# Kernel optimization log

Measured on AMD Instinct MI355X. Metric: run time of the kernel, lower is better.

## Reference

```python
import jax, jax.numpy as jnp
import numpy as np

NEG_INF = -1.0e9  # matches masked_fill value in the torch source


def setup_inputs() -> dict:
    key = jax.random.key(0)
    k1, k2, k3, k4 = jax.random.split(key, 4)
    B, H, L, D = 4, 16, 2048, 64
    query = jax.random.normal(k1, (B, H, L, D), dtype=jnp.float32)
    key_t = jax.random.normal(k2, (B, H, L, D), dtype=jnp.float32)
    value = jax.random.normal(k3, (B, H, L, D), dtype=jnp.float32)
    attention_mask = jax.random.randint(k4, (B, L), 0, 2, dtype=jnp.int64)
    return {"query": query, "key": key_t, "value": value, "attention_mask": attention_mask}


def reference(query, key, value, attention_mask):
    d = query.shape[-1]
    scale = 1.0 / jnp.sqrt(jnp.asarray(d, dtype=query.dtype))
    # scores: [B, H, Lq, Lk]
    scores = jnp.einsum("bhqd,bhkd->bhqk", query, key) * scale
    # mask: [B, Lk] -> [B, 1, 1, Lk]; positions where mask == 0 get -1e9
    m = attention_mask[:, None, None, :]
    scores = jnp.where(m == 0, jnp.asarray(NEG_INF, dtype=scores.dtype), scores)
    attn = jax.nn.softmax(scores, axis=-1)
    return jnp.einsum("bhqk,bhkd->bhqd", attn, value)
```

## Files before the change

### kernel.cpp

```cpp
#include <hip/hip_runtime.h>
#include <hip/hip_bf16.h>
#include <stdint.h>

#define B_    4
#define H_    16
#define L_    2048
#define D_    64
#define BH_   64
#define NT_   32
#define MASKBIAS (-1.4426950408889634e9f)

typedef __attribute__((ext_vector_type(8))) short bf16x8;
typedef __attribute__((ext_vector_type(8))) unsigned short ushort8;
typedef __attribute__((ext_vector_type(4))) unsigned short ushort4v;
typedef __attribute__((ext_vector_type(4))) float f32x4;

__device__ __forceinline__ ushort f2bf(float f) {
  union { float f; uint32_t u; } x; x.f = f;
  uint32_t r = x.u + 0x7FFFu + ((x.u >> 16) & 1u);
  return (ushort)(r >> 16);
}

__device__ __forceinline__ uint32_t pkbf(float lo, float hi) {
  uint32_t r;
  asm("v_cvt_pk_bf16_f32 %0, %1, %2" : "=v"(r) : "v"(lo), "v"(hi));
  return r;
}

__global__ __launch_bounds__(256, 2)
void prep_kv(const float* __restrict__ K, const float* __restrict__ V,
             const int* __restrict__ Mask,
             ushort* __restrict__ Kp, ushort* __restrict__ Vtp,
             float* __restrict__ Mb)
{
  __shared__ ushort Vl[64 * 68];
  const int bid = blockIdx.x;
  const int tid = threadIdx.x;
  const float* Kg = K + (size_t)bid * 4096;
  const float* Vg = V + (size_t)bid * 4096;
  ushort* Kt = Kp + (size_t)bid * 4096;
  ushort* Vt = Vtp + (size_t)bid * 4096;

#pragma unroll
  for (int j = 0; j < 2; ++j) {
    int chunk = j * 256 + tid;
    int row = chunk >> 3, d8 = chunk & 7;
    const float* s = Kg + row * 64 + d8 * 8;
    float4 a = *(const float4*)s, b2 = *(const float4*)(s + 4);
    ushort8 o;
    o[0]=f2bf(a.x); o[1]=f2bf(a.y); o[2]=f2bf(a.z); o[3]=f2bf(a.w);
    o[4]=f2bf(b2.x);o[5]=f2bf(b2.y);o[6]=f2bf(b2.z);o[7]=f2bf(b2.w);
    *(ushort8*)(Kt + row * 64 + ((d8 * 8) ^ ((row & 7) << 3))) = o;

    const float* sv = Vg + row * 64 + d8 * 8;
    float4 va = *(const float4*)sv, vb2 = *(const float4*)(sv + 4);
    ushort4v w0, w1;
    w0[0]=f2bf(va.x); w0[1]=f2bf(va.y); w0[2]=f2bf(va.z); w0[3]=f2bf(va.w);
    w1[0]=f2bf(vb2.x);w1[1]=f2bf(vb2.y);w1[2]=f2bf(vb2.z);w1[3]=f2bf(vb2.w);
    *(ushort4v*)(&Vl[row * 68 + d8 * 8])     = w0;
    *(ushort4v*)(&Vl[row * 68 + d8 * 8 + 4]) = w1;
  }
  __syncthreads();
#pragma unroll
  for (int j = 0; j < 2; ++j) {
    int chunk = j * 256 + tid;
    int d = chunk >> 3, p8 = chunk & 7;
    ushort8 o;
#pragma unroll
    for (int e = 0; e < 8; ++e) {
      int pos = p8 * 8 + e;
      int c = pos >> 5, lgv = (pos >> 3) & 3, bb = (pos >> 2) & 1, aa = pos & 3;
      int kk = 32 * c + 16 * bb + 4 * lgv + aa;
      o[e] = Vl[kk * 68 + d];
    }
    *(ushort8*)(Vt + d * 64 + ((p8 * 8) ^ ((d & 7) << 3))) = o;
  }
  if ((((bid >> 5) & 15) == 0) && tid < 64) {
    int b = bid >> 9, kt = bid & 31;
    int idx = b * 2048 + kt * 64 + tid;
    Mb[idx] = (Mask[idx] != 0) ? 0.f : MASKBIAS;
  }
}

__global__ __launch_bounds__(256, 2)
void attn_fwd13(const float* __restrict__ Q, const float* __restrict__ Mb,
                const ushort* __restrict__ Kp, const ushort* __restrict__ Vtp,
                float* __restrict__ O)
{
  __shared__ __align__(16) ushort Kb[2][4096];
  __shared__ __align__(16) ushort Vb[2][4096];

  const int tid  = threadIdx.x;
  const int wid  = tid >> 6;
  const int lane = tid & 63;
  const int lr   = lane & 15;
  const int lg   = lane >> 4;

  const int x   = blockIdx.x;
  const int lin = (x & 7) * 64 + (x >> 3);
  const int bh  = lin >> 3;
  const int qt  = lin & 7;
  const int b   = bh >> 4;

  const int phase = ((x >> 8) & 1) << 4;

  const float*  Qg    = Q + (size_t)bh * L_ * D_;
  float*        Og    = O + (size_t)bh * L_ * D_;
  const ushort* Kbase = Kp  + (size_t)bh * 131072;
  const ushort* Vbase = Vtp + (size_t)bh * 131072;
  const float*  Mbb   = Mb + (size_t)b * L_;

  const int qbase = qt * 256 + wid * 64;
  const float qscale = 0.125f * 1.4426950408889634f;

  bf16x8 qf[4][2];
#pragma unroll
  for (int g = 0; g < 4; ++g)
#pragma unroll
    for (int c = 0; c < 2; ++c) {
      const float* src = Qg + (size_t)(qbase + g * 16 + lr) * D_ + c * 32 + lg * 8;
      float4 a = *(const float4*)src, b2 = *(const float4*)(src + 4);
      bf16x8 q;
      q[0]=f2bf(a.x*qscale);  q[1]=f2bf(a.y*qscale);  q[2]=f2bf(a.z*qscale);  q[3]=f2bf(a.w*qscale);
      q[4]=f2bf(b2.x*qscale); q[5]=f2bf(b2.y*qscale); q[6]=f2bf(b2.z*qscale); q[7]=f2bf(b2.w*qscale);
      qf[g][c] = q;
    }

  f32x4 o_acc[4][4];
#pragma unroll
  for (int g = 0; g < 4; ++g)
#pragma unroll
    for (int dt = 0; dt < 4; ++dt) o_acc[g][dt] = (f32x4){0.f,0.f,0.f,0.f};
  f32x4 l4[4];
#pragma unroll
  for (int g = 0; g < 4; ++g) l4[g] = (f32x4){0.f,0.f,0.f,0.f};

  int kts = phase;
  ushort8 rk0, rk1, rv0, rv1;
  rk0 = *(const ushort8*)(Kbase + (size_t)kts * 4096 + wid * 1024 + lane * 8);
  rk1 = *(const ushort8*)(Kbase + (size_t)kts * 4096 + wid * 1024 + 512 + lane * 8);
  rv0 = *(const ushort8*)(Vbase + (size_t)kts * 4096 + wid * 1024 + lane * 8);
  rv1 = *(const ushort8*)(Vbase + (size_t)kts * 4096 + wid * 1024 + 512 + lane * 8);

  int cur = 0;
  for (int kt = 0; kt < NT_; ++kt) {
    *(ushort8*)(&Kb[cur][wid * 1024 + lane * 8])       = rk0;
    *(ushort8*)(&Kb[cur][wid * 1024 + 512 + lane * 8]) = rk1;
    *(ushort8*)(&Vb[cur][wid * 1024 + lane * 8])       = rv0;
    *(ushort8*)(&Vb[cur][wid * 1024 + 512 + lane * 8]) = rv1;

    __syncthreads();

    const int knx = (kts + 1) & 31;
    {
      const ushort* Ks = Kbase + (size_t)knx * 4096;
      const ushort* Vs = Vbase + (size_t)knx * 4096;
      rk0 = *(const ushort8*)(Ks + wid * 1024 + lane * 8);
      rk1 = *(const ushort8*)(Ks + wid * 1024 + 512 + lane * 8);
      rv0 = *(const ushort8*)(Vs + wid * 1024 + lane * 8);
      rv1 = *(const ushort8*)(Vs + wid * 1024 + 512 + lane * 8);
    }

    f32x4 bt[4];
#pragma unroll
    for (int t = 0; t < 4; ++t) bt[t] = *(const f32x4*)(Mbb + kts * 64 + 16 * t + 4 * lg);

    const ushort* Kc = Kb[cur];
    const ushort* Vc = Vb[cur];

    bf16x8 kf[4][2], vb[4][2];
#pragma unroll
    for (int t = 0; t < 4; ++t)
#pragma unroll
      for (int c = 0; c < 2; ++c) {
        kf[t][c] = *(const bf16x8*)(Kc + (16 * t + lr) * 64 + ((c * 32 + lg * 8) ^ ((lr & 7) << 3)));
        vb[t][c] = *(const bf16x8*)(Vc + (16 * t + lr) * 64 + ((c * 32 + lg * 8) ^ ((lr & 7) << 3)));
      }

#pragma unroll
    for (int g = 0; g < 4; ++g) {
      f32x4 st[4];
      __builtin_amdgcn_s_setprio(1);
#pragma unroll
      for (int t = 0; t < 4; ++t)
        st[t] = __builtin_amdgcn_mfma_f32_16x16x32_bf16(kf[t][0], qf[g][0], bt[t], 0, 0, 0);
#pragma unroll
      for (int t = 0; t < 4; ++t)
        st[t] = __builtin_amdgcn_mfma_f32_16x16x32_bf16(kf[t][1], qf[g][1], st[t], 0, 0, 0);
      __builtin_amdgcn_s_setprio(0);

      f32x4 p0, p1, p2, p3;
#pragma unroll
      for (int r = 0; r < 4; ++r) {
        p0[r] = __builtin_amdgcn_exp2f(st[0][r]);
        p1[r] = __builtin_amdgcn_exp2f(st[1][r]);
        p2[r] = __builtin_amdgcn_exp2f(st[2][r]);
        p3[r] = __builtin_amdgcn_exp2f(st[3][r]);
      }
      l4[g] += (p0 + p1) + (p2 + p3);

      union PKU { uint32_t u[8]; bf16x8 v[2]; } pk;
      pk.u[0] = pkbf(p0[0], p0[1]); pk.u[1] = pkbf(p0[2], p0[3]);
      pk.u[2] = pkbf(p1[0], p1[1]); pk.u[3] = pkbf(p1[2], p1[3]);
      pk.u[4] = pkbf(p2[0], p2[1]); pk.u[5] = pkbf(p2[2], p2[3]);
      pk.u[6] = pkbf(p3[0], p3[1]); pk.u[7] = pkbf(p3[2], p3[3]);

      __builtin_amdgcn_s_setprio(1);
#pragma unroll
      for (int c = 0; c < 2; ++c)
#pragma unroll
        for (int dt = 0; dt < 4; ++dt)
          o_acc[g][dt] = __builtin_amdgcn_mfma_f32_16x16x32_bf16(pk.v[c], vb[dt][c], o_acc[g][dt], 0, 0, 0);
      __builtin_amdgcn_s_setprio(0);
    }

    kts = knx;
    cur ^= 1;
  }

#pragma unroll
  for (int g = 0; g < 4; ++g) {
    float lsum = (l4[g][0] + l4[g][1]) + (l4[g][2] + l4[g][3]);
    lsum += __shfl_xor(lsum, 16);
    lsum += __shfl_xor(lsum, 32);
    float linv[4];
#pragma unroll
    for (int r = 0; r < 4; ++r) {
      float lq = __shfl(lsum, 20 * lg + r);
      linv[r] = 1.0f / lq;
    }
#pragma unroll
    for (int dt = 0; dt < 4; ++dt)
#pragma unroll
      for (int r = 0; r < 4; ++r) {
        int row = qbase + g * 16 + 4 * lg + r;
        Og[(size_t)row * D_ + dt * 16 + lr] = o_acc[g][dt][r] * linv[r];
      }
  }
}

extern "C" void kernel_launch(void* const* d_in, const int* in_sizes, int n_in,
                              void* d_out, int out_size, void* d_ws, size_t ws_size,
                              hipStream_t stream) {
  const float* Q = (const float*)d_in[0];
  const float* K = (const float*)d_in[1];
  const float* V = (const float*)d_in[2];
  const int*   M = (const int*)d_in[3];
  float*       O = (float*)d_out;

  const size_t elems = (size_t)BH_ * L_ * D_;
  ushort* Kp  = (ushort*)d_ws;
  ushort* Vtp = Kp + elems;
  float*  Mb  = (float*)(Vtp + elems);
  prep_kv<<<dim3(BH_ * NT_), dim3(256), 0, stream>>>(K, V, M, Kp, Vtp, Mb);
  attn_fwd13<<<dim3(512), dim3(256), 0, stream>>>(Q, Mb, Kp, Vtp, O);
}
```

Baseline: 97.09 us.

## Switch attention MFMAs from 16x16x32 to 32x32x16 tiles with new V layout

Rewrites the attention kernel so QK^T and PV both use 32x32x16 bf16 MFMA instructions instead of 16x16x32. The V-transpose layout in the prep kernel and the Q, K, P fragment mappings change to match the 32x32 operand layout. The PV product now runs after both query groups' P tiles are built, and V fragments are loaded from LDS inside that loop. The aim is fewer MFMA issues and more operand reuse per instruction, at the cost of more accumulator registers and new LDS access patterns that may conflict on banks.

```diff
diff --git a/kernel.cpp b/kernel.cpp
--- a/kernel.cpp
+++ b/kernel.cpp
@@ -14,6 +14,7 @@
 typedef __attribute__((ext_vector_type(8))) unsigned short ushort8;
 typedef __attribute__((ext_vector_type(4))) unsigned short ushort4v;
 typedef __attribute__((ext_vector_type(4))) float f32x4;
+typedef __attribute__((ext_vector_type(16))) float f32x16;
 
 __device__ __forceinline__ ushort f2bf(float f) {
   union { float f; uint32_t u; } x; x.f = f;
@@ -64,16 +65,17 @@
 #pragma unroll
   for (int j = 0; j < 2; ++j) {
     int chunk = j * 256 + tid;
-    int d = chunk >> 3, p8 = chunk & 7;
+    int sh = chunk & 1;
+    int d  = (chunk >> 1) & 63;
+    int c  = (chunk >> 7) & 1;
+    int h  = (chunk >> 8) & 1;
     ushort8 o;
 #pragma unroll
     for (int e = 0; e < 8; ++e) {
-      int pos = p8 * 8 + e;
-      int c = pos >> 5, lgv = (pos >> 3) & 3, bb = (pos >> 2) & 1, aa = pos & 3;
-      int kk = 32 * c + 16 * bb + 4 * lgv + aa;
-      o[e] = Vl[kk * 68 + d];
-    }
-    *(ushort8*)(Vt + d * 64 + ((p8 * 8) ^ ((d & 7) << 3))) = o;
+      int k = (e & 3) + 4 * sh + 8 * (e >> 2) + 16 * c + 32 * h;
+      o[e] = Vl[k * 68 + d];
+    }
+    *(ushort8*)(Vt + ((h * 2 + c) * 64 + d) * 16 + sh * 8) = o;
   }
   if ((((bid >> 5) & 15) == 0) && tid < 64) {
     int b = bid >> 9, kt = bid & 31;
@@ -83,7 +85,7 @@
 }
 
 __global__ __launch_bounds__(256, 2)
-void attn_fwd13(const float* __restrict__ Q, const float* __restrict__ Mb,
+void attn_fwd14(const float* __restrict__ Q, const float* __restrict__ Mb,
                 const ushort* __restrict__ Kp, const ushort* __restrict__ Vtp,
                 float* __restrict__ O)
 {
@@ -93,8 +95,8 @@
   const int tid  = threadIdx.x;
   const int wid  = tid >> 6;
   const int lane = tid & 63;
-  const int lr   = lane & 15;
-  const int lg   = lane >> 4;
+  const int lq   = lane & 31;
+  const int hi   = lane >> 5;
 
   const int x   = blockIdx.x;
   const int lin = (x & 7) * 64 + (x >> 3);
@@ -113,27 +115,29 @@
   const int qbase = qt * 256 + wid * 64;
   const float qscale = 0.125f * 1.4426950408889634f;
 
-  bf16x8 qf[4][2];
-#pragma unroll
-  for (int g = 0; g < 4; ++g)
-#pragma unroll
-    for (int c = 0; c < 2; ++c) {
-      const float* src = Qg + (size_t)(qbase + g * 16 + lr) * D_ + c * 32 + lg * 8;
+  bf16x8 qf[2][4];
+#pragma unroll
+  for (int g = 0; g < 2; ++g)
+#pragma unroll
+    for (int s = 0; s < 4; ++s) {
+      const float* src = Qg + (size_t)(qbase + g * 32 + lq) * D_ + s * 16 + hi * 8;
       float4 a = *(const float4*)src, b2 = *(const float4*)(src + 4);
       bf16x8 q;
       q[0]=f2bf(a.x*qscale);  q[1]=f2bf(a.y*qscale);  q[2]=f2bf(a.z*qscale);  q[3]=f2bf(a.w*qscale);
       q[4]=f2bf(b2.x*qscale); q[5]=f2bf(b2.y*qscale); q[6]=f2bf(b2.z*qscale); q[7]=f2bf(b2.w*qscale);
-      qf[g][c] = q;
-    }
-
-  f32x4 o_acc[4][4];
-#pragma unroll
-  for (int g = 0; g < 4; ++g)
-#pragma unroll
-    for (int dt = 0; dt < 4; ++dt) o_acc[g][dt] = (f32x4){0.f,0.f,0.f,0.f};
-  f32x4 l4[4];
-#pragma unroll
-  for (int g = 0; g < 4; ++g) l4[g] = (f32x4){0.f,0.f,0.f,0.f};
+      qf[g][s] = q;
+    }
+
+  f32x16 o_acc[2][2];
+#pragma unroll
+  for (int g = 0; g < 2; ++g)
+#pragma unroll
+    for (int dh = 0; dh < 2; ++dh)
+#pragma unroll
+      for (int r = 0; r < 16; ++r) o_acc[g][dh][r] = 0.f;
+  f32x4 l4[2];
+#pragma unroll
+  for (int g = 0; g < 2; ++g) l4[g] = (f32x4){0.f,0.f,0.f,0.f};
 
   int kts = phase;
   ushort8 rk0, rk1, rv0, rv1;
@@ -161,81 +165,99 @@
       rv1 = *(const ushort8*)(Vs + wid * 1024 + 512 + lane * 8);
     }
 
-    f32x4 bt[4];
-#pragma unroll
-    for (int t = 0; t < 4; ++t) bt[t] = *(const f32x4*)(Mbb + kts * 64 + 16 * t + 4 * lg);
+    f32x16 bt[2];
+#pragma unroll
+    for (int h = 0; h < 2; ++h)
+#pragma unroll
+      for (int rq = 0; rq < 4; ++rq) {
+        f32x4 t = *(const f32x4*)(Mbb + kts * 64 + 32 * h + 8 * rq + 4 * hi);
+#pragma unroll
+        for (int j = 0; j < 4; ++j) bt[h][rq * 4 + j] = t[j];
+      }
 
     const ushort* Kc = Kb[cur];
     const ushort* Vc = Vb[cur];
 
-    bf16x8 kf[4][2], vb[4][2];
-#pragma unroll
-    for (int t = 0; t < 4; ++t)
-#pragma unroll
-      for (int c = 0; c < 2; ++c) {
-        kf[t][c] = *(const bf16x8*)(Kc + (16 * t + lr) * 64 + ((c * 32 + lg * 8) ^ ((lr & 7) << 3)));
-        vb[t][c] = *(const bf16x8*)(Vc + (16 * t + lr) * 64 + ((c * 32 + lg * 8) ^ ((lr & 7) << 3)));
-      }
-
-#pragma unroll
-    for (int g = 0; g < 4; ++g) {
-      f32x4 st[4];
+    bf16x8 kf[2][4];
+#pragma unroll
+    for (int h = 0; h < 2; ++h)
+#pragma unroll
+      for (int s = 0; s < 4; ++s)
+        kf[h][s] = *(const bf16x8*)(Kc + (lq + 32 * h) * 64 + ((s * 16 + hi * 8) ^ ((lq & 7) << 3)));
+
+    union PK2 { uint32_t u[8]; bf16x8 v[2]; } pkg[2][2];
+#pragma unroll
+    for (int g = 0; g < 2; ++g) {
+      f32x16 st0 = bt[0], st1 = bt[1];
       __builtin_amdgcn_s_setprio(1);
 #pragma unroll
-      for (int t = 0; t < 4; ++t)
-        st[t] = __builtin_amdgcn_mfma_f32_16x16x32_bf16(kf[t][0], qf[g][0], bt[t], 0, 0, 0);
-#pragma unroll
-      for (int t = 0; t < 4; ++t)
-        st[t] = __builtin_amdgcn_mfma_f32_16x16x32_bf16(kf[t][1], qf[g][1], st[t], 0, 0, 0);
+      for (int s = 0; s < 4; ++s)
+        st0 = __builtin_amdgcn_mfma_f32_32x32x16_bf16(kf[0][s], qf[g][s], st0, 0, 0, 0);
+#pragma unroll
+      for (int s = 0; s < 4; ++s)
+        st1 = __builtin_amdgcn_mfma_f32_32x32x16_bf16(kf[1][s], qf[g][s], st1, 0, 0, 0);
       __builtin_amdgcn_s_setprio(0);
 
-      f32x4 p0, p1, p2, p3;
-#pragma unroll
-      for (int r = 0; r < 4; ++r) {
-        p0[r] = __builtin_amdgcn_exp2f(st[0][r]);
-        p1[r] = __builtin_amdgcn_exp2f(st[1][r]);
-        p2[r] = __builtin_amdgcn_exp2f(st[2][r]);
-        p3[r] = __builtin_amdgcn_exp2f(st[3][r]);
-      }
-      l4[g] += (p0 + p1) + (p2 + p3);
-
-      union PKU { uint32_t u[8]; bf16x8 v[2]; } pk;
-      pk.u[0] = pkbf(p0[0], p0[1]); pk.u[1] = pkbf(p0[2], p0[3]);
-      pk.u[2] = pkbf(p1[0], p1[1]); pk.u[3] = pkbf(p1[2], p1[3]);
-      pk.u[4] = pkbf(p2[0], p2[1]); pk.u[5] = pkbf(p2[2], p2[3]);
-      pk.u[6] = pkbf(p3[0], p3[1]); pk.u[7] = pkbf(p3[2], p3[3]);
-
-      __builtin_amdgcn_s_setprio(1);
+      float p0[16], p1[16];
+#pragma unroll
+      for (int r = 0; r < 16; ++r) {
+        p0[r] = __builtin_amdgcn_exp2f(st0[r]);
+        p1[r] = __builtin_amdgcn_exp2f(st1[r]);
+      }
+#pragma unroll
+      for (int rq = 0; rq < 4; ++rq)
+#pragma unroll
+        for (int j = 0; j < 4; ++j)
+          l4[g][j] += p0[rq * 4 + j] + p1[rq * 4 + j];
 #pragma unroll
       for (int c = 0; c < 2; ++c)
 #pragma unroll
-        for (int dt = 0; dt < 4; ++dt)
-          o_acc[g][dt] = __builtin_amdgcn_mfma_f32_16x16x32_bf16(pk.v[c], vb[dt][c], o_acc[g][dt], 0, 0, 0);
-      __builtin_amdgcn_s_setprio(0);
-    }
+        for (int jw = 0; jw < 4; ++jw) {
+          pkg[g][0].u[c * 4 + jw] = pkbf(p0[8 * c + 2 * jw], p0[8 * c + 2 * jw + 1]);
+          pkg[g][1].u[c * 4 + jw] = pkbf(p1[8 * c + 2 * jw], p1[8 * c + 2 * jw + 1]);
+        }
+    }
+
+    __builtin_amdgcn_s_setprio(1);
+#pragma unroll
+    for (int kc = 0; kc < 4; ++kc) {
+      const int h = kc >> 1, c = kc & 1;
+#pragma unroll
+      for (int dh = 0; dh < 2; ++dh) {
+        bf16x8 vbf = *(const bf16x8*)(Vc + (kc * 64 + lq + 32 * dh) * 16 + hi * 8);
+#pragma unroll
+        for (int g = 0; g < 2; ++g)
+          o_acc[g][dh] = __builtin_amdgcn_mfma_f32_32x32x16_bf16(pkg[g][h].v[c], vbf, o_acc[g][dh], 0, 0, 0);
+      }
+    }
+    __builtin_amdgcn_s_setprio(0);
 
     kts = knx;
     cur ^= 1;
   }
 
 #pragma unroll
-  for (int g = 0; g < 4; ++g) {
+  for (int g = 0; g < 2; ++g) {
     float lsum = (l4[g][0] + l4[g][1]) + (l4[g][2] + l4[g][3]);
-    lsum += __shfl_xor(lsum, 16);
     lsum += __shfl_xor(lsum, 32);
-    float linv[4];
-#pragma unroll
-    for (int r = 0; r < 4; ++r) {
-      float lq = __shfl(lsum, 20 * lg + r);
-      linv[r] = 1.0f / lq;
-    }
-#pragma unroll
-    for (int dt = 0; dt < 4; ++dt)
-#pragma unroll
-      for (int r = 0; r < 4; ++r) {
-        int row = qbase + g * 16 + 4 * lg + r;
-        Og[(size_t)row * D_ + dt * 16 + lr] = o_acc[g][dt][r] * linv[r];
-      }
+    float lv[16];
+#pragma unroll
+    for (int rq = 0; rq < 4; ++rq)
+#pragma unroll
+      for (int j = 0; j < 4; ++j) {
+        int row = j + 8 * rq + 4 * hi;
+        lv[rq * 4 + j] = 1.0f / __shfl(lsum, row);
+      }
+#pragma unroll
+    for (int dh = 0; dh < 2; ++dh)
+#pragma unroll
+      for (int rq = 0; rq < 4; ++rq)
+#pragma unroll
+        for (int j = 0; j < 4; ++j) {
+          int row = j + 8 * rq + 4 * hi;
+          Og[(size_t)(qbase + g * 32 + row) * D_ + dh * 32 + lq] =
+              o_acc[g][dh][rq * 4 + j] * lv[rq * 4 + j];
+        }
   }
 }
 
@@ -253,5 +275,5 @@
   ushort* Vtp = Kp + elems;
   float*  Mb  = (float*)(Vtp + elems);
   prep_kv<<<dim3(BH_ * NT_), dim3(256), 0, stream>>>(K, V, M, Kp, Vtp, Mb);
-  attn_fwd13<<<dim3(512), dim3(256), 0, stream>>>(Q, Mb, Kp, Vtp, O);
-}
+  attn_fwd14<<<dim3(512), dim3(256), 0, stream>>>(Q, Mb, Kp, Vtp, O);
+}
```

Result: slower. 99.66 us (+2.6%).
